# Performance work log

Hardware: AMD Instinct MI355X
Metric: run time of the kernel (lower is better)

## Reference

```python
import jax, jax.numpy as jnp
import numpy as np

B, N, C = 64, 256, 512
SHIFTS = (-1, 0, 1)
# torch.chunk(N, 3): ceil(256/3)=86 -> sizes [86, 86, 84]
CHUNK_SIZES = (86, 86, 84)
EPS = 1e-5


def _shift_pad(a, s):
    # shift along last axis (C) with zero padding, matching shift_with_padding
    if s == 0:
        return a
    if s > 0:
        return jnp.pad(a[..., :-s], ((0, 0), (0, 0), (s, 0)))
    s = -s
    return jnp.pad(a[..., s:], ((0, 0), (0, 0), (0, s)))


def setup_inputs() -> dict:
    key = jax.random.key(0)
    ks = jax.random.split(key, 16)
    w = lambda k, shape: (jax.random.normal(k, shape, jnp.float32) * 0.02)
    inp = {
        "x": jax.random.normal(ks[0], (B, N, C), jnp.float32),
        "ln_g": jnp.ones((C,), jnp.float32),
        "ln_b": jnp.zeros((C,), jnp.float32),
        "Ws": w(ks[1], (C, C)),
        "bs": jnp.zeros((C,), jnp.float32),
        "Wc": w(ks[2], (N, N, 3)),     # Conv1d weight [out=N, in=N, k=3]
        "bc": jnp.zeros((N,), jnp.float32),
        "We1": w(ks[3], (N, N // 8)),
        "be1": jnp.zeros((N // 8,), jnp.float32),
        "We2": w(ks[4], (N // 8, N)),
        "be2": jnp.zeros((N,), jnp.float32),
        "Wf1": w(ks[5], (C, 2 * C)),
        "bf1": jnp.zeros((2 * C,), jnp.float32),
        "Wf2": w(ks[6], (2 * C, C)),
        "bf2": jnp.zeros((C,), jnp.float32),
    }
    return inp


def reference(x, ln_g, ln_b, Ws, bs, Wc, bc, We1, be1, We2, be2, Wf1, bf1, Wf2, bf2):
    res = x
    # channel_mixer_S: LayerNorm over C, then Linear C->C + relu (dropout=0)
    mu = jnp.mean(x, axis=-1, keepdims=True)
    var = jnp.mean((x - mu) ** 2, axis=-1, keepdims=True)
    h = (x - mu) * jax.lax.rsqrt(var + EPS) * ln_g + ln_b
    h = jax.nn.relu(h @ Ws + bs)                      # [B, N, C]
    # channel_shift: chunk along N, shift each chunk along C with zero pad
    offs = np.cumsum((0,) + CHUNK_SIZES)
    chunks = [h[:, offs[i]:offs[i + 1], :] for i in range(3)]
    x_shift = jnp.concatenate([_shift_pad(c, s) for c, s in zip(chunks, SHIFTS)], axis=1)
    # channel_projection: Conv1d over C with N channels, k=3, pad=1
    x_shift = jax.lax.conv_general_dilated(
        x_shift, Wc, window_strides=(1,), padding=[(1, 1)],
        dimension_numbers=("NCH", "OIH", "NCH")) + bc[None, :, None]
    # SE gating
    se = jnp.mean(x_shift, axis=-1)                   # [B, N]
    ex = jax.nn.sigmoid(jax.nn.relu(se @ We1 + be1) @ We2 + be2)  # [B, N]
    z = x_shift * ex[:, :, None]
    # channel_mixer_F: C -> 2C (relu) -> C, residual
    z = jax.nn.relu(z @ Wf1 + bf1) @ Wf2 + bf2 + res
    return z
```

## Files before the change

### kernel.cpp

```cpp
#include <hip/hip_runtime.h>
#include <hip/hip_bf16.h>
#include <math.h>

#define BB 64
#define NN 256
#define CCH 512

typedef unsigned short u16;
typedef __attribute__((ext_vector_type(8))) short s16x8;
typedef __attribute__((ext_vector_type(4))) float f32x4;

#define AS1 __attribute__((address_space(1)))
#define AS3 __attribute__((address_space(3)))

static __device__ __forceinline__ u16 f2b(float f) {
    __hip_bfloat16 h = __float2bfloat16(f);
    union { __hip_bfloat16 h; u16 u; } x; x.h = h; return x.u;
}
static __device__ __forceinline__ void gll16(const void* g, void* l) {
    __builtin_amdgcn_global_load_lds((const AS1 unsigned int*)g,
                                     (AS3 unsigned int*)l, 16, 0, 0);
}

#define VM8  asm volatile("s_waitcnt vmcnt(8)" ::: "memory")
#define VM6  asm volatile("s_waitcnt vmcnt(6)" ::: "memory")
#define VM0  asm volatile("s_waitcnt vmcnt(0)" ::: "memory")
#define LGKM0 asm volatile("s_waitcnt lgkmcnt(0)" ::: "memory")
#define MEMB asm volatile("" ::: "memory")

static __device__ __forceinline__ void wtc_body(const float* __restrict__ W,
    u16* __restrict__ Wt, int K, int N, int bx, int by, float* t )
{
    int n0 = bx * 32, k0 = by * 32;
    int tx = threadIdx.x & 31, ty = threadIdx.x >> 5;
    #pragma unroll
    for (int i = 0; i < 4; ++i)
        t[(ty + i * 8) * 33 + tx] = W[(size_t)(k0 + ty + i * 8) * N + n0 + tx];
    __syncthreads();
    #pragma unroll
    for (int i = 0; i < 4; ++i)
        Wt[(size_t)(n0 + ty + i * 8) * K + k0 + tx] = f2b(t[tx * 33 + ty + i * 8]);
}

__global__ __launch_bounds__(256) void prep_ln_kernel(
    const float* __restrict__ Ws,  u16* __restrict__ Wst,
    const float* __restrict__ Wf1, u16* __restrict__ Wf1t,
    const float* __restrict__ Wf2, u16* __restrict__ Wf2t,
    const float* __restrict__ Wc,  u16* __restrict__ Wc3,
    u16* __restrict__ Hts,
    const float* __restrict__ x, const float* __restrict__ g,
    const float* __restrict__ bta, u16* __restrict__ xnorm)
{
    __shared__ float t[32 * 33];
    int bid = blockIdx.x;
    if (bid < 256) {
        wtc_body(Ws, Wst, 512, 512, bid & 15, bid >> 4, t);
    } else if (bid < 768) {
        int idx = bid - 256;
        wtc_body(Wf1, Wf1t, 512, 1024, idx & 31, idx >> 5, t);
    } else if (bid < 1280) {
        int idx = bid - 768;
        wtc_body(Wf2, Wf2t, 1024, 512, idx & 15, idx >> 4, t);
    } else if (bid < 2048) {
        int idx = (bid - 1280) * 256 + threadIdx.x;
        int i = idx & 255;
        int o = (idx >> 8) & 255;
        int k = idx >> 16;
        Wc3[idx] = f2b(Wc[((size_t)o * NN + i) * 3 + k]);
    } else if (bid < 2304) {
        int idx = (bid - 2048) * 256 + threadIdx.x;
        int b   = idx >> 10;
        int rem = idx & 1023;
        int rr  = rem >> 8;
        int r   = (rr & 1) + (rr >> 1) * 512;
        Hts[((size_t)b * 514 + r) * 256 + (rem & 255)] = 0;
    } else {
        const int l = threadIdx.x & 63;
        const int r = (bid - 2304) * 4 + (threadIdx.x >> 6);
        const float4* xr = (const float4*)(x + (size_t)r * CCH);
        float4 v1 = xr[l];
        float4 v2 = xr[l + 64];
        float s  = v1.x + v1.y + v1.z + v1.w + v2.x + v2.y + v2.z + v2.w;
        float ss = v1.x*v1.x + v1.y*v1.y + v1.z*v1.z + v1.w*v1.w
                 + v2.x*v2.x + v2.y*v2.y + v2.z*v2.z + v2.w*v2.w;
        #pragma unroll
        for (int o = 32; o > 0; o >>= 1) {
            s  += __shfl_xor(s, o);
            ss += __shfl_xor(ss, o);
        }
        float mu  = s * (1.0f / CCH);
        float var = ss * (1.0f / CCH) - mu * mu;
        float rs  = rsqrtf(var + 1e-5f);
        float4 g1 = ((const float4*)g)[l],   g2 = ((const float4*)g)[l + 64];
        float4 b1 = ((const float4*)bta)[l], b2 = ((const float4*)bta)[l + 64];
        ushort4 o1, o2;
        o1.x = f2b((v1.x - mu) * rs * g1.x + b1.x);
        o1.y = f2b((v1.y - mu) * rs * g1.y + b1.y);
        o1.z = f2b((v1.z - mu) * rs * g1.z + b1.z);
        o1.w = f2b((v1.w - mu) * rs * g1.w + b1.w);
        o2.x = f2b((v2.x - mu) * rs * g2.x + b2.x);
        o2.y = f2b((v2.y - mu) * rs * g2.y + b2.y);
        o2.z = f2b((v2.z - mu) * rs * g2.z + b2.z);
        o2.w = f2b((v2.w - mu) * rs * g2.w + b2.w);
        ushort4* orow = (ushort4*)(xnorm + (size_t)r * CCH);
        orow[l]      = o1;
        orow[l + 64] = o2;
    }
}

template<int MODE>
__global__ __launch_bounds__(512, 1) void gemm_pipe(
    const u16* __restrict__ A, const u16* __restrict__ Bt,
    const float* __restrict__ bias, const float* __restrict__ res,
    void* __restrict__ outv, u16* __restrict__ auxout,
    float* __restrict__ SEpart)
{
    constexpr int NK = (MODE == 2) ? 32 : (MODE == 3) ? 24 : 16;
    constexpr int SA = (MODE == 2) ? 1024 : 512;
    constexpr int SB = (MODE == 2) ? 1024 : 512;
    constexpr int NOUT = 512;

    __shared__ u16 Asm[6 * 8192];
    __shared__ u16 Bsm[6 * 4096];

    const int tid = threadIdx.x;
    const int l   = tid & 63;
    const int w   = tid >> 6;
    const int nwg = gridDim.x;
    const int work = (blockIdx.x & 7) * (nwg >> 3) + (blockIdx.x >> 3);

    int row0, col0, bidx = 0;
    if (MODE == 0)      { row0 = (work >> 7) * 256; col0 = (work & 127) * 128; }
    else if (MODE == 2) { row0 = (work >> 2) * 256; col0 = (work & 3) * 128; }
    else                { row0 = 0; bidx = work >> 2; col0 = (work & 3) * 128; }

    const u16* Aab  = A + (size_t)row0 * SA;
    const u16* Bab  = Bt + (size_t)col0 * SB;
    const u16* HtsB = Bt + (size_t)bidx * 514 * 256;

    const int wm = (w >> 2) * 128;
    const int wn = (w & 3) * 32;
    const int fr = l & 15;
    const int q  = l >> 4;
    const int kofs = ((q ^ ((l >> 1) & 3)) * 8);

    const f32x4 zero = {0.0f, 0.0f, 0.0f, 0.0f};
    f32x4 acc[8][2];
    #pragma unroll
    for (int m = 0; m < 8; ++m) { acc[m][0] = zero; acc[m][1] = zero; }

    const int kc0 = ((tid & 3) ^ ((tid >> 3) & 3)) * 8;
    const int srow = tid >> 2;

    auto stage = [&](int u, int slot) {
        u16* ald = Asm + slot * 8192 + w * 512;
        u16* bld = Bsm + slot * 4096 + w * 512;
        if (MODE == 3) {
            const int kseg = u >> 3, kb = (u & 7) * 32 + kc0;
            gll16(A + kseg * 65536 + srow * 256 + kb, ald);
            gll16(A + kseg * 65536 + (srow + 128) * 256 + kb, ald + 4096);
            gll16(HtsB + (size_t)(col0 + srow + kseg) * 256 + kb, bld);
        } else {
            const int kb = u * 32 + kc0;
            gll16(Aab + (size_t)srow * SA + kb, ald);
            gll16(Aab + (size_t)(srow + 128) * SA + kb, ald + 4096);
            gll16(Bab + (size_t)srow * SB + kb, bld);
        }
    };

    stage(0, 0); stage(1, 1); stage(2, 2); stage(3, 3);
    int sa = 0;
    constexpr int NV = NK / 2;
    for (int v = 0; v < NV; ++v) {
        if (v + 1 < NV) { VM6; } else { VM0; }
        __builtin_amdgcn_s_barrier();
        MEMB;
        const int sb = sa + 1;
        s16x8 b0[2], af0[8];
        #pragma unroll
        for (int n = 0; n < 2; ++n)
            b0[n] = *(const s16x8*)&Bsm[sa * 4096 + (wn + n * 16 + fr) * 32 + kofs];
        #pragma unroll
        for (int m = 0; m < 8; ++m)
            af0[m] = *(const s16x8*)&Asm[sa * 8192 + (wm + m * 16 + fr) * 32 + kofs];
        const int u2 = 2 * v + 4;
        if (u2 < NK) {
            int st = sa + 4; if (st >= 6) st -= 6;
            stage(u2, st);
            int st1 = st + 1; if (st1 >= 6) st1 -= 6;
            stage(u2 + 1, st1);
        }
        __builtin_amdgcn_s_setprio(1);
        #pragma unroll
        for (int m = 0; m < 8; ++m)
            #pragma unroll
            for (int n = 0; n < 2; ++n)
                acc[m][n] = __builtin_amdgcn_mfma_f32_16x16x32_bf16(af0[m], b0[n], acc[m][n], 0, 0, 0);
        __builtin_amdgcn_s_setprio(0);
        s16x8 b1[2], af1[8];
        #pragma unroll
        for (int n = 0; n < 2; ++n)
            b1[n] = *(const s16x8*)&Bsm[sb * 4096 + (wn + n * 16 + fr) * 32 + kofs];
        #pragma unroll
        for (int m = 0; m < 8; ++m)
            af1[m] = *(const s16x8*)&Asm[sb * 8192 + (wm + m * 16 + fr) * 32 + kofs];
        __builtin_amdgcn_s_setprio(1);
        #pragma unroll
        for (int m = 0; m < 8; ++m)
            #pragma unroll
            for (int n = 0; n < 2; ++n)
                acc[m][n] = __builtin_amdgcn_mfma_f32_16x16x32_bf16(af1[m], b1[n], acc[m][n], 0, 0, 0);
        __builtin_amdgcn_s_setprio(0);
        MEMB;
        sa += 2; if (sa >= 6) sa = 0;
    }

    if (MODE == 0) {
        #pragma unroll
        for (int m = 0; m < 8; ++m) {
            #pragma unroll
            for (int j = 0; j < 4; ++j) {
                const int c = row0 + wm + m * 16 + (l >> 4) * 4 + j;
                const float bsv = bias[c];
                #pragma unroll
                for (int n = 0; n < 2; ++n) {
                    const int gcol = col0 + wn + n * 16 + fr;
                    const int b  = gcol >> 8;
                    const int ni = gcol & 255;
                    const int s  = (ni < 86) ? -1 : (ni < 172 ? 0 : 1);
                    auxout[((size_t)b * 514 + c + 1 + s) * 256 + ni] =
                        f2b(fmaxf(acc[m][n][j] + bsv, 0.0f));
                }
            }
        }
    } else if (MODE == 2) {
        #pragma unroll
        for (int m = 0; m < 8; ++m) {
            #pragma unroll
            for (int j = 0; j < 4; ++j) {
                const int row = row0 + wm + m * 16 + (l >> 4) * 4 + j;
                #pragma unroll
                for (int n = 0; n < 2; ++n) {
                    const int col = col0 + wn + n * 16 + fr;
                    ((float*)outv)[(size_t)row * NOUT + col] =
                        acc[m][n][j] + bias[col] + res[(size_t)row * NOUT + col];
                }
            }
        }
    } else {
        const int ct = col0 >> 7;
        #pragma unroll
        for (int m = 0; m < 8; ++m) {
            #pragma unroll
            for (int j = 0; j < 4; ++j) {
                const int no = wm + m * 16 + (l >> 4) * 4 + j;
                const float bcv = bias[no];
                float p = 0.0f;
                #pragma unroll
                for (int n = 0; n < 2; ++n) {
                    const int c = col0 + wn + n * 16 + fr;
                    float v = acc[m][n][j];
                    auxout[((size_t)bidx * NN + no) * CCH + c] = f2b(v + bcv);
                    p += v;
                }
                p += __shfl_xor(p, 1);
                p += __shfl_xor(p, 2);
                p += __shfl_xor(p, 4);
                p += __shfl_xor(p, 8);
                if (fr == 0)
                    SEpart[ct * 16384 + bidx * NN + no] = p;
            }
        }
    }
}

__global__ __launch_bounds__(512, 1) void gemm1_8ph(
    const u16* __restrict__ Yb, const u16* __restrict__ Wf1t,
    const float* __restrict__ bf1, u16* __restrict__ T,
    const float* __restrict__ SEpart, const float* __restrict__ bc,
    const float* __restrict__ We1, const float* __restrict__ be1,
    const float* __restrict__ We2, const float* __restrict__ be2)
{
    __shared__ u16 Ab[2][256 * 64];
    __shared__ u16 Bb[2][256 * 64];
    __shared__ float sse[256];
    __shared__ float e1f[32];
    __shared__ float exs[256];

    const int tid = threadIdx.x;
    const int l   = tid & 63;
    const int w   = tid >> 6;
    const int work = (blockIdx.x & 7) * 32 + (blockIdx.x >> 3);
    const int row0 = (work >> 2) * 256;
    const int col0 = (work & 3) * 256;

    const u16* Aab = Yb  + (size_t)row0 * 512;
    const u16* Bab = Wf1t + (size_t)col0 * 512;

    const int wm = (w >> 2) * 128;
    const int wn = (w & 3) * 64;
    const int fr = l & 15;
    const int q  = l >> 4;
    const int r7 = fr & 7;

    if (tid < 256) {
        int o = row0 + tid;
        sse[tid] = (SEpart[o] + SEpart[16384 + o] + SEpart[32768 + o]
                    + SEpart[49152 + o]) * (1.0f / CCH) + bc[tid];
    }
    __syncthreads();
    if (tid < 32) {
        float a = be1[tid];
        #pragma unroll 8
        for (int i = 0; i < 256; ++i) a += sse[i] * We1[i * 32 + tid];
        e1f[tid] = fmaxf(a, 0.0f);
    }
    __syncthreads();
    if (tid < 256) {
        float a = be2[tid];
        #pragma unroll
        for (int j = 0; j < 32; ++j) a += e1f[j] * We2[j * 256 + tid];
        exs[tid] = 1.0f / (1.0f + expf(-a));
    }
    __syncthreads();

    const int strow = tid >> 3;
    const int sslot = tid & 7;
    const int gslot = sslot ^ (strow & 7);
    const size_t goff = (size_t)strow * 512 + gslot * 8;
    const int     loff = strow * 64 + sslot * 8;

    auto stageA = [&](int c, int kt, int j) {
        gll16(Aab + (size_t)(j * 64) * 512 + kt * 64 + goff,
              &Ab[c][j * 64 * 64 + loff]);
    };
    auto stageB = [&](int c, int kt, int j) {
        gll16(Bab + (size_t)(j * 64) * 512 + kt * 64 + goff,
              &Bb[c][j * 64 * 64 + loff]);
    };

    stageA(0, 0, 0); stageA(0, 0, 1); stageA(0, 0, 2); stageA(0, 0, 3);
    stageB(0, 0, 0); stageB(0, 0, 1); stageB(0, 0, 2); stageB(0, 0, 3);
    stageA(1, 1, 0); stageA(1, 1, 2);
    stageB(1, 1, 0); stageB(1, 1, 1); stageB(1, 1, 2); stageB(1, 1, 3);

    const f32x4 zero = {0.0f, 0.0f, 0.0f, 0.0f};
    f32x4 acc[8][4];
    #pragma unroll
    for (int m = 0; m < 8; ++m)
        #pragma unroll
        for (int n = 0; n < 4; ++n) acc[m][n] = zero;

    s16x8 afv[4][2], bfv[4][2];

#define LDA8(c, r, ks) (*(const s16x8*)&Ab[c][(r) * 64 + (((((ks) << 2) + q) ^ r7) << 3)])
#define LDB8(c, r, ks) (*(const s16x8*)&Bb[c][(r) * 64 + (((((ks) << 2) + q) ^ r7) << 3)])

    for (int t = 0; t < 8; ++t) {
        const int c = t & 1;
        if (t < 7) { stageA(c ^ 1, t + 1, 1); stageA(c ^ 1, t + 1, 3); VM8; }
        else       { VM0; }
        __builtin_amdgcn_s_barrier();
        MEMB;
        #pragma unroll
        for (int m = 0; m < 4; ++m) {
            afv[m][0] = LDA8(c, wm + m * 16 + fr, 0);
            afv[m][1] = LDA8(c, wm + m * 16 + fr, 1);
        }
        #pragma unroll
        for (int n = 0; n < 2; ++n) {
            bfv[n][0] = LDB8(c, wn + n * 16 + fr, 0);
            bfv[n][1] = LDB8(c, wn + n * 16 + fr, 1);
        }
        LGKM0;
        __builtin_amdgcn_s_setprio(1);
        #pragma unroll
        for (int m = 0; m < 4; ++m)
            #pragma unroll
            for (int n = 0; n < 2; ++n) {
                acc[m][n] = __builtin_amdgcn_mfma_f32_16x16x32_bf16(afv[m][0], bfv[n][0], acc[m][n], 0, 0, 0);
                acc[m][n] = __builtin_amdgcn_mfma_f32_16x16x32_bf16(afv[m][1], bfv[n][1], acc[m][n], 0, 0, 0);
            }
        __builtin_amdgcn_s_setprio(0);
        __builtin_amdgcn_s_barrier();
        if (t < 6) { stageA(c, t + 2, 0); stageA(c, t + 2, 2); }
        #pragma unroll
        for (int n = 2; n < 4; ++n) {
            bfv[n][0] = LDB8(c, wn + n * 16 + fr, 0);
            bfv[n][1] = LDB8(c, wn + n * 16 + fr, 1);
        }
        LGKM0;
        __builtin_amdgcn_s_setprio(1);
        #pragma unroll
        for (int m = 0; m < 4; ++m)
            #pragma unroll
            for (int n = 2; n < 4; ++n) {
                acc[m][n] = __builtin_amdgcn_mfma_f32_16x16x32_bf16(afv[m][0], bfv[n][0], acc[m][n], 0, 0, 0);
                acc[m][n] = __builtin_amdgcn_mfma_f32_16x16x32_bf16(afv[m][1], bfv[n][1], acc[m][n], 0, 0, 0);
            }
        __builtin_amdgcn_s_setprio(0);
        __builtin_amdgcn_s_barrier();
        if (t < 6) { stageB(c, t + 2, 0); stageB(c, t + 2, 1); }
        #pragma unroll
        for (int m = 0; m < 4; ++m) {
            afv[m][0] = LDA8(c, wm + 64 + m * 16 + fr, 0);
            afv[m][1] = LDA8(c, wm + 64 + m * 16 + fr, 1);
        }
        LGKM0;
        __builtin_amdgcn_s_setprio(1);
        #pragma unroll
        for (int m = 0; m < 4; ++m)
            #pragma unroll
            for (int n = 0; n < 2; ++n) {
                acc[4 + m][n] = __builtin_amdgcn_mfma_f32_16x16x32_bf16(afv[m][0], bfv[n][0], acc[4 + m][n], 0, 0, 0);
                acc[4 + m][n] = __builtin_amdgcn_mfma_f32_16x16x32_bf16(afv[m][1], bfv[n][1], acc[4 + m][n], 0, 0, 0);
            }
        __builtin_amdgcn_s_setprio(0);
        __builtin_amdgcn_s_barrier();
        if (t < 6) { stageB(c, t + 2, 2); stageB(c, t + 2, 3); }
        __builtin_amdgcn_s_setprio(1);
        #pragma unroll
        for (int m = 0; m < 4; ++m)
            #pragma unroll
            for (int n = 2; n < 4; ++n) {
                acc[4 + m][n] = __builtin_amdgcn_mfma_f32_16x16x32_bf16(afv[m][0], bfv[n][0], acc[4 + m][n], 0, 0, 0);
                acc[4 + m][n] = __builtin_amdgcn_mfma_f32_16x16x32_bf16(afv[m][1], bfv[n][1], acc[4 + m][n], 0, 0, 0);
            }
        __builtin_amdgcn_s_setprio(0);
        __builtin_amdgcn_s_barrier();
    }

    #pragma unroll
    for (int m = 0; m < 8; ++m) {
        #pragma unroll
        for (int j = 0; j < 4; ++j) {
            const int rl  = wm + m * 16 + q * 4 + j;
            const int row = row0 + rl;
            const float sc = exs[rl];
            #pragma unroll
            for (int n = 0; n < 4; ++n) {
                const int col = col0 + wn + n * 16 + fr;
                T[(size_t)row * 1024 + col] =
                    f2b(fmaxf(acc[m][n][j] * sc + bf1[col], 0.0f));
            }
        }
    }
#undef LDA8
#undef LDB8
}

extern "C" void kernel_launch(void* const* d_in, const int* in_sizes, int n_in,
                              void* d_out, int out_size, void* d_ws, size_t ws_size,
                              hipStream_t stream) {
    const float* x    = (const float*)d_in[0];
    const float* ln_g = (const float*)d_in[1];
    const float* ln_b = (const float*)d_in[2];
    const float* Ws   = (const float*)d_in[3];
    const float* bs   = (const float*)d_in[4];
    const float* Wc   = (const float*)d_in[5];
    const float* bc   = (const float*)d_in[6];
    const float* We1  = (const float*)d_in[7];
    const float* be1  = (const float*)d_in[8];
    const float* We2  = (const float*)d_in[9];
    const float* be2  = (const float*)d_in[10];
    const float* Wf1  = (const float*)d_in[11];
    const float* bf1  = (const float*)d_in[12];
    const float* Wf2  = (const float*)d_in[13];
    const float* bf2  = (const float*)d_in[14];
    float* out = (float*)d_out;
    char* w8   = (char*)d_ws;

    u16* XN  = (u16*)(w8);
    u16* Y   = XN;
    u16* Hts = (u16*)(w8 + (16u << 20));
    u16* T   = (u16*)(w8 + (16u << 20));
    char* tail = w8 + 50397184;
    float* SEpart = (float*)(tail);
    u16* Wst      = (u16*)(tail + 262144);
    u16* Wf1t     = (u16*)(tail + 786432);
    u16* Wf2t     = (u16*)(tail + 1835008);
    u16* Wc3      = (u16*)(tail + 2883584);

    prep_ln_kernel<<<6400, 256, 0, stream>>>(Ws, Wst, Wf1, Wf1t, Wf2, Wf2t,
                                             Wc, Wc3, Hts, x, ln_g, ln_b, XN);
    gemm_pipe<0><<<256, 512, 0, stream>>>(Wst, XN, bs, nullptr,
                                          nullptr, Hts, nullptr);
    gemm_pipe<3><<<256, 512, 0, stream>>>(Wc3, Hts, bc, nullptr,
                                          nullptr, Y, SEpart);
    gemm1_8ph<<<256, 512, 0, stream>>>(Y, Wf1t, bf1, T, SEpart, bc,
                                       We1, be1, We2, be2);
    gemm_pipe<2><<<256, 512, 0, stream>>>(T, Wf2t, bf2, x,
                                          out, nullptr, nullptr);
}
```

Baseline: 116.6 us.

## Use 64x64 warp tiles and permute K so epilogues store vectorized ushort4

Changes the per-warp tile in gemm_pipe from 128x32 to 64x64. It also permutes the K/column order of the bf16 weight copies (Wf1t, Wf2t, Wc3) so that each lane's four MFMA output columns are contiguous in memory. This lets the epilogues of the Ws GEMM, the conv GEMM and gemm1 write ushort4 vectors instead of scattered 2-byte stores. SE partial sums grow from 4 to 8 slots, so the workspace offsets shift. The square warp tile changes LDS fragment reuse and register use, and correctness depends on the permutations lining up across all stages.

Result: no change. 114.4 us, median of 2 (-1.8%).

```diff
diff --git a/kernel.cpp b/kernel.cpp
--- a/kernel.cpp
+++ b/kernel.cpp
@@ -20,6 +20,9 @@
 static __device__ __forceinline__ void gll16(const void* g, void* l) {
     __builtin_amdgcn_global_load_lds((const AS1 unsigned int*)g,
                                      (AS3 unsigned int*)l, 16, 0, 0);
+}
+static __device__ __forceinline__ int shf(int ni) {
+    return (ni < 86) ? -1 : (ni < 172 ? 0 : 1);
 }
 
 #define VM8  asm volatile("s_waitcnt vmcnt(8)" ::: "memory")
@@ -29,7 +32,7 @@
 #define MEMB asm volatile("" ::: "memory")
 
 static __device__ __forceinline__ void wtc_body(const float* __restrict__ W,
-    u16* __restrict__ Wt, int K, int N, int bx, int by, float* t )
+    u16* __restrict__ Wt, int K, int N, int bx, int by, float* t, bool perm)
 {
     int n0 = bx * 32, k0 = by * 32;
     int tx = threadIdx.x & 31, ty = threadIdx.x >> 5;
@@ -37,9 +40,11 @@
     for (int i = 0; i < 4; ++i)
         t[(ty + i * 8) * 33 + tx] = W[(size_t)(k0 + ty + i * 8) * N + n0 + tx];
     __syncthreads();
+    int kl = k0 + tx;
+    int kp = perm ? ((kl & ~63) | ((kl & 15) << 2) | ((kl >> 4) & 3)) : kl;
     #pragma unroll
     for (int i = 0; i < 4; ++i)
-        Wt[(size_t)(n0 + ty + i * 8) * K + k0 + tx] = f2b(t[tx * 33 + ty + i * 8]);
+        Wt[(size_t)(n0 + ty + i * 8) * K + kp] = f2b(t[tx * 33 + ty + i * 8]);
 }
 
 __global__ __launch_bounds__(256) void prep_ln_kernel(
@@ -54,19 +59,20 @@
     __shared__ float t[32 * 33];
     int bid = blockIdx.x;
     if (bid < 256) {
-        wtc_body(Ws, Wst, 512, 512, bid & 15, bid >> 4, t);
+        wtc_body(Ws, Wst, 512, 512, bid & 15, bid >> 4, t, false);
     } else if (bid < 768) {
         int idx = bid - 256;
-        wtc_body(Wf1, Wf1t, 512, 1024, idx & 31, idx >> 5, t);
+        wtc_body(Wf1, Wf1t, 512, 1024, idx & 31, idx >> 5, t, true);
     } else if (bid < 1280) {
         int idx = bid - 768;
-        wtc_body(Wf2, Wf2t, 1024, 512, idx & 15, idx >> 4, t);
+        wtc_body(Wf2, Wf2t, 1024, 512, idx & 15, idx >> 4, t, true);
     } else if (bid < 2048) {
         int idx = (bid - 1280) * 256 + threadIdx.x;
-        int i = idx & 255;
+        int xloc = idx & 255;
         int o = (idx >> 8) & 255;
         int k = idx >> 16;
-        Wc3[idx] = f2b(Wc[((size_t)o * NN + i) * 3 + k]);
+        int il = (xloc & ~63) | ((xloc & 63) >> 2) | ((xloc & 3) << 4);
+        Wc3[idx] = f2b(Wc[((size_t)o * NN + il) * 3 + k]);
     } else if (bid < 2304) {
         int idx = (bid - 2048) * 256 + threadIdx.x;
         int b   = idx >> 10;
@@ -118,7 +124,6 @@
     constexpr int NK = (MODE == 2) ? 32 : (MODE == 3) ? 24 : 16;
     constexpr int SA = (MODE == 2) ? 1024 : 512;
     constexpr int SB = (MODE == 2) ? 1024 : 512;
-    constexpr int NOUT = 512;
 
     __shared__ u16 Asm[6 * 8192];
     __shared__ u16 Bsm[6 * 4096];
@@ -138,16 +143,18 @@
     const u16* Bab  = Bt + (size_t)col0 * SB;
     const u16* HtsB = Bt + (size_t)bidx * 514 * 256;
 
-    const int wm = (w >> 2) * 128;
-    const int wn = (w & 3) * 32;
+    const int wm = (w >> 1) * 64;
+    const int wn = (w & 1) * 64;
     const int fr = l & 15;
     const int q  = l >> 4;
     const int kofs = ((q ^ ((l >> 1) & 3)) * 8);
 
     const f32x4 zero = {0.0f, 0.0f, 0.0f, 0.0f};
-    f32x4 acc[8][2];
+    f32x4 acc[4][4];
     #pragma unroll
-    for (int m = 0; m < 8; ++m) { acc[m][0] = zero; acc[m][1] = zero; }
+    for (int m = 0; m < 4; ++m)
+        #pragma unroll
+        for (int n = 0; n < 4; ++n) acc[m][n] = zero;
 
     const int kc0 = ((tid & 3) ^ ((tid >> 3) & 3)) * 8;
     const int srow = tid >> 2;
@@ -176,12 +183,12 @@
         __builtin_amdgcn_s_barrier();
         MEMB;
         const int sb = sa + 1;
-        s16x8 b0[2], af0[8];
-        #pragma unroll
-        for (int n = 0; n < 2; ++n)
+        s16x8 b0[4], af0[4];
+        #pragma unroll
+        for (int n = 0; n < 4; ++n)
             b0[n] = *(const s16x8*)&Bsm[sa * 4096 + (wn + n * 16 + fr) * 32 + kofs];
         #pragma unroll
-        for (int m = 0; m < 8; ++m)
+        for (int m = 0; m < 4; ++m)
             af0[m] = *(const s16x8*)&Asm[sa * 8192 + (wm + m * 16 + fr) * 32 + kofs];
         const int u2 = 2 * v + 4;
         if (u2 < NK) {
@@ -192,23 +199,23 @@
         }
         __builtin_amdgcn_s_setprio(1);
         #pragma unroll
-        for (int m = 0; m < 8; ++m)
-            #pragma unroll
-            for (int n = 0; n < 2; ++n)
+        for (int m = 0; m < 4; ++m)
+            #pragma unroll
+            for (int n = 0; n < 4; ++n)
                 acc[m][n] = __builtin_amdgcn_mfma_f32_16x16x32_bf16(af0[m], b0[n], acc[m][n], 0, 0, 0);
         __builtin_amdgcn_s_setprio(0);
-        s16x8 b1[2], af1[8];
-        #pragma unroll
-        for (int n = 0; n < 2; ++n)
+        s16x8 b1[4], af1[4];
+        #pragma unroll
+        for (int n = 0; n < 4; ++n)
             b1[n] = *(const s16x8*)&Bsm[sb * 4096 + (wn + n * 16 + fr) * 32 + kofs];
         #pragma unroll
-        for (int m = 0; m < 8; ++m)
+        for (int m = 0; m < 4; ++m)
             af1[m] = *(const s16x8*)&Asm[sb * 8192 + (wm + m * 16 + fr) * 32 + kofs];
         __builtin_amdgcn_s_setprio(1);
         #pragma unroll
-        for (int m = 0; m < 8; ++m)
-            #pragma unroll
-            for (int n = 0; n < 2; ++n)
+        for (int m = 0; m < 4; ++m)
+            #pragma unroll
+            for (int n = 0; n < 4; ++n)
                 acc[m][n] = __builtin_amdgcn_mfma_f32_16x16x32_bf16(af1[m], b1[n], acc[m][n], 0, 0, 0);
         __builtin_amdgcn_s_setprio(0);
         MEMB;
@@ -216,59 +223,73 @@
     }
 
     if (MODE == 0) {
-        #pragma unroll
-        for (int m = 0; m < 8; ++m) {
+        const int gb = col0 + wn;
+        const int b  = gb >> 8;
+        const int gl = gb & 255;
+        const int nib = gl + fr;
+        u16* HtsW = auxout + (size_t)b * 514 * 256;
+        const int px = gl + 4 * fr;
+        const int s0 = shf(nib), s3 = shf(nib + 48);
+        #pragma unroll
+        for (int m = 0; m < 4; ++m) {
             #pragma unroll
             for (int j = 0; j < 4; ++j) {
-                const int c = row0 + wm + m * 16 + (l >> 4) * 4 + j;
+                const int c = row0 + wm + m * 16 + q * 4 + j;
                 const float bsv = bias[c];
+                u16 vv[4];
                 #pragma unroll
-                for (int n = 0; n < 2; ++n) {
-                    const int gcol = col0 + wn + n * 16 + fr;
-                    const int b  = gcol >> 8;
-                    const int ni = gcol & 255;
-                    const int s  = (ni < 86) ? -1 : (ni < 172 ? 0 : 1);
-                    auxout[((size_t)b * 514 + c + 1 + s) * 256 + ni] =
-                        f2b(fmaxf(acc[m][n][j] + bsv, 0.0f));
+                for (int n = 0; n < 4; ++n)
+                    vv[n] = f2b(fmaxf(acc[m][n][j] + bsv, 0.0f));
+                if (s0 == s3) {
+                    ushort4 v4 = {vv[0], vv[1], vv[2], vv[3]};
+                    *(ushort4*)&HtsW[(size_t)(c + 1 + s0) * 256 + px] = v4;
+                } else {
+                    #pragma unroll
+                    for (int n = 0; n < 4; ++n)
+                        HtsW[(size_t)(c + 1 + shf(nib + n * 16)) * 256 + px + n] = vv[n];
                 }
             }
         }
     } else if (MODE == 2) {
         #pragma unroll
-        for (int m = 0; m < 8; ++m) {
+        for (int m = 0; m < 4; ++m) {
             #pragma unroll
             for (int j = 0; j < 4; ++j) {
-                const int row = row0 + wm + m * 16 + (l >> 4) * 4 + j;
+                const int row = row0 + wm + m * 16 + q * 4 + j;
                 #pragma unroll
-                for (int n = 0; n < 2; ++n) {
+                for (int n = 0; n < 4; ++n) {
                     const int col = col0 + wn + n * 16 + fr;
-                    ((float*)outv)[(size_t)row * NOUT + col] =
-                        acc[m][n][j] + bias[col] + res[(size_t)row * NOUT + col];
+                    ((float*)outv)[(size_t)row * 512 + col] =
+                        acc[m][n][j] + bias[col] + res[(size_t)row * 512 + col];
                 }
             }
         }
     } else {
-        const int ct = col0 >> 7;
-        #pragma unroll
-        for (int m = 0; m < 8; ++m) {
+        const int cb = col0 + wn;
+        const int px = cb + 4 * fr;
+        const int sslot = (col0 >> 7) * 2 + (wn >> 6);
+        #pragma unroll
+        for (int m = 0; m < 4; ++m) {
             #pragma unroll
             for (int j = 0; j < 4; ++j) {
-                const int no = wm + m * 16 + (l >> 4) * 4 + j;
+                const int no = wm + m * 16 + q * 4 + j;
                 const float bcv = bias[no];
                 float p = 0.0f;
+                u16 vv[4];
                 #pragma unroll
-                for (int n = 0; n < 2; ++n) {
-                    const int c = col0 + wn + n * 16 + fr;
+                for (int n = 0; n < 4; ++n) {
                     float v = acc[m][n][j];
-                    auxout[((size_t)bidx * NN + no) * CCH + c] = f2b(v + bcv);
+                    vv[n] = f2b(v + bcv);
                     p += v;
                 }
+                ushort4 v4 = {vv[0], vv[1], vv[2], vv[3]};
+                *(ushort4*)&auxout[((size_t)bidx * NN + no) * CCH + px] = v4;
                 p += __shfl_xor(p, 1);
                 p += __shfl_xor(p, 2);
                 p += __shfl_xor(p, 4);
                 p += __shfl_xor(p, 8);
                 if (fr == 0)
-                    SEpart[ct * 16384 + bidx * NN + no] = p;
+                    SEpart[sslot * 16384 + bidx * NN + no] = p;
             }
         }
     }
@@ -305,8 +326,10 @@
 
     if (tid < 256) {
         int o = row0 + tid;
-        sse[tid] = (SEpart[o] + SEpart[16384 + o] + SEpart[32768 + o]
-                    + SEpart[49152 + o]) * (1.0f / CCH) + bc[tid];
+        float sum = 0.0f;
+        #pragma unroll
+        for (int i = 0; i < 8; ++i) sum += SEpart[i * 16384 + o];
+        sse[tid] = sum * (1.0f / CCH) + bc[tid];
     }
     __syncthreads();
     if (tid < 32) {
@@ -430,6 +453,10 @@
         __builtin_amdgcn_s_barrier();
     }
 
+    const int cgb = col0 + wn;
+    float bval[4];
+    #pragma unroll
+    for (int n = 0; n < 4; ++n) bval[n] = bf1[cgb + n * 16 + fr];
     #pragma unroll
     for (int m = 0; m < 8; ++m) {
         #pragma unroll
@@ -437,12 +464,12 @@
             const int rl  = wm + m * 16 + q * 4 + j;
             const int row = row0 + rl;
             const float sc = exs[rl];
-            #pragma unroll
-            for (int n = 0; n < 4; ++n) {
-                const int col = col0 + wn + n * 16 + fr;
-                T[(size_t)row * 1024 + col] =
-                    f2b(fmaxf(acc[m][n][j] * sc + bf1[col], 0.0f));
-            }
+            u16 vv[4];
+            #pragma unroll
+            for (int n = 0; n < 4; ++n)
+                vv[n] = f2b(fmaxf(acc[m][n][j] * sc + bval[n], 0.0f));
+            ushort4 v4 = {vv[0], vv[1], vv[2], vv[3]};
+            *(ushort4*)&T[(size_t)row * 1024 + cgb + 4 * fr] = v4;
         }
     }
 #undef LDA8
@@ -476,10 +503,10 @@
     u16* T   = (u16*)(w8 + (16u << 20));
     char* tail = w8 + 50397184;
     float* SEpart = (float*)(tail);
-    u16* Wst      = (u16*)(tail + 262144);
-    u16* Wf1t     = (u16*)(tail + 786432);
-    u16* Wf2t     = (u16*)(tail + 1835008);
-    u16* Wc3      = (u16*)(tail + 2883584);
+    u16* Wst      = (u16*)(tail + 524288);
+    u16* Wf1t     = (u16*)(tail + 1048576);
+    u16* Wf2t     = (u16*)(tail + 2097152);
+    u16* Wc3      = (u16*)(tail + 3145728);
 
     prep_ln_kernel<<<6400, 256, 0, stream>>>(Ws, Wst, Wf1, Wf1t, Wf2, Wf2t,
                                              Wc, Wc3, Hts, x, ln_g, ln_b, XN);
```
